# Performance work log

Measured on AMD Instinct MI355X. Metric: run time of the kernel, lower is better.

The kernel has to match this reference:

```python
import jax, jax.numpy as jnp
import numpy as np

N_PROP = 2048
N_CLS = 81  # background + 80 foreground classes
IMG_W, IMG_H = 1333.0, 800.0
SCORE_THRESH = 0.05
NMS_THRESH = 0.5
DET_PER_IMG = 100
BBOX_CLIP = float(np.log(1000.0 / 16.0))
TO_REMOVE = 1.0


def setup_inputs() -> dict:
    key = jax.random.key(0)
    k1, k2, k3, k4, k5, k6 = jax.random.split(key, 6)
    class_logits = jax.random.normal(k1, (N_PROP, N_CLS), jnp.float32)
    box_regression = jax.random.normal(k2, (N_PROP, N_CLS * 4), jnp.float32)
    # valid xyxy proposals inside the image
    x1 = jax.random.uniform(k3, (N_PROP,), jnp.float32, 0.0, IMG_W * 0.7)
    y1 = jax.random.uniform(k4, (N_PROP,), jnp.float32, 0.0, IMG_H * 0.7)
    w = jax.random.uniform(k5, (N_PROP,), jnp.float32, 16.0, IMG_W * 0.3)
    h = jax.random.uniform(k6, (N_PROP,), jnp.float32, 16.0, IMG_H * 0.3)
    proposals = jnp.stack([x1, y1, x1 + w, y1 + h], axis=-1)
    return {"class_logits": class_logits, "box_regression": box_regression, "proposals": proposals}


def decode_boxes(reg, props):
    # BoxCoder.decode with weights (10,10,5,5); reg: [N, C*4] -> [N, C, 4]
    widths = props[:, 2] - props[:, 0] + TO_REMOVE
    heights = props[:, 3] - props[:, 1] + TO_REMOVE
    ctr_x = props[:, 0] + 0.5 * widths
    ctr_y = props[:, 1] + 0.5 * heights
    r = reg.reshape(reg.shape[0], -1, 4)
    dx = r[..., 0] / 10.0
    dy = r[..., 1] / 10.0
    dw = jnp.minimum(r[..., 2] / 5.0, BBOX_CLIP)
    dh = jnp.minimum(r[..., 3] / 5.0, BBOX_CLIP)
    pcx = dx * widths[:, None] + ctr_x[:, None]
    pcy = dy * heights[:, None] + ctr_y[:, None]
    pw = jnp.exp(dw) * widths[:, None]
    ph = jnp.exp(dh) * heights[:, None]
    return jnp.stack([pcx - 0.5 * pw, pcy - 0.5 * ph,
                      pcx + 0.5 * pw - TO_REMOVE, pcy + 0.5 * ph - TO_REMOVE], axis=-1)


def pairwise_iou(b):
    # b: [N,4] xyxy -> [N,N] IoU with +1 pixel convention
    area = (b[:, 2] - b[:, 0] + TO_REMOVE) * (b[:, 3] - b[:, 1] + TO_REMOVE)
    lt = jnp.maximum(b[:, None, :2], b[None, :, :2])
    rb = jnp.minimum(b[:, None, 2:], b[None, :, 2:])
    wh = jnp.clip(rb - lt + TO_REMOVE, 0.0)
    inter = wh[..., 0] * wh[..., 1]
    return inter / (area[:, None] + area[None, :] - inter)


def nms_keep(boxes, scores, valid, thresh):
    # returns boolean keep mask (fixed shape) equivalent to greedy NMS on valid boxes
    n = scores.shape[0]
    order = jnp.argsort(-scores)
    b = boxes[order]
    v = valid[order]
    iou = pairwise_iou(b)  # [N,N]
    idx = jnp.arange(n)

    def step(suppressed, inp):
        row, vi, i = inp
        keep_i = vi & jnp.logical_not(suppressed[i])
        suppressed = suppressed | (keep_i & (row > thresh) & (idx > i))
        return suppressed, keep_i

    _, keep_sorted = jax.lax.scan(step, jnp.zeros(n, bool), (iou, v, idx))
    return jnp.zeros(n, bool).at[order].set(keep_sorted)


def _forward(class_logits, box_regression, proposals):
    probs = jax.nn.softmax(class_logits, axis=-1)          # [N, C]
    boxes = decode_boxes(box_regression, proposals)        # [N, C, 4]
    # clip_to_image (remove_empty=False)
    boxes = jnp.stack([jnp.clip(boxes[..., 0], 0.0, IMG_W - TO_REMOVE),
                       jnp.clip(boxes[..., 1], 0.0, IMG_H - TO_REMOVE),
                       jnp.clip(boxes[..., 2], 0.0, IMG_W - TO_REMOVE),
                       jnp.clip(boxes[..., 3], 0.0, IMG_H - TO_REMOVE)], axis=-1)
    # drop background class 0; class-major layout [C-1, N, ...]
    boxes_c = jnp.transpose(boxes[:, 1:, :], (1, 0, 2))    # [C-1, N, 4]
    scores_c = probs[:, 1:].T                              # [C-1, N]
    valid = scores_c > SCORE_THRESH
    keep = jax.vmap(nms_keep, in_axes=(0, 0, 0, None))(boxes_c, scores_c, valid, NMS_THRESH)
    masked = jnp.where(keep, scores_c, -1.0)               # invalid -> below any prob
    flat_scores = masked.reshape(-1)                       # [(C-1)*N]
    _, top_idx = jax.lax.top_k(flat_scores, DET_PER_IMG)
    out_scores = flat_scores[top_idx]
    out_boxes = boxes_c.reshape(-1, 4)[top_idx]
    out_labels = top_idx // N_PROP + 1                     # class labels in [1, C-1]
    return out_boxes, out_scores, out_labels


def reference(class_logits, box_regression, proposals):
    return _forward(class_logits, box_regression, proposals)
```

## Files before the change

### kernel.cpp

```cpp
#include <hip/hip_runtime.h>
#include <math.h>

#define NPROP 2048
#define NCLS 81
#define NFG 80
#define CAP 512
#define TOPC 100
#define CPAD 16
#define NB 1152
#define BMIN 0x7A99


#define LDS_FENCE() do { __builtin_amdgcn_wave_barrier(); \
    asm volatile("s_waitcnt lgkmcnt(0)" ::: "memory");     \
    __builtin_amdgcn_wave_barrier(); } while (0)

__device__ __forceinline__ void decode_clip(const float* __restrict__ props,
                                            const float* __restrict__ reg,
                                            int p, int cls, float out[4]) {
    float px1 = props[p * 4 + 0], py1 = props[p * 4 + 1];
    float px2 = props[p * 4 + 2], py2 = props[p * 4 + 3];
    float w = px2 - px1 + 1.0f;
    float h = py2 - py1 + 1.0f;
    float cx = px1 + 0.5f * w;
    float cy = py1 + 0.5f * h;
    const float* r = reg + (size_t)p * (NCLS * 4) + cls * 4;
    float dx = r[0] / 10.0f;
    float dy = r[1] / 10.0f;
    float dw = fminf(r[2] / 5.0f, 4.135166556742356f);
    float dh = fminf(r[3] / 5.0f, 4.135166556742356f);
    float pcx = dx * w + cx;
    float pcy = dy * h + cy;
    float pw = expf(dw) * w;
    float ph = expf(dh) * h;
    float x1 = pcx - 0.5f * pw;
    float y1 = pcy - 0.5f * ph;
    float x2 = pcx + 0.5f * pw - 1.0f;
    float y2 = pcy + 0.5f * ph - 1.0f;
    out[0] = fminf(fmaxf(x1, 0.0f), 1332.0f);
    out[1] = fminf(fmaxf(y1, 0.0f), 799.0f);
    out[2] = fminf(fmaxf(x2, 0.0f), 1332.0f);
    out[3] = fminf(fmaxf(y2, 0.0f), 799.0f);
}

__global__ __launch_bounds__(256) void softmax_scatter(const float* __restrict__ logits,
                                                       int* __restrict__ ccnt,
                                                       unsigned long long* __restrict__ cand) {
    int gw = (blockIdx.x * blockDim.x + threadIdx.x) >> 6;
    int lane = threadIdx.x & 63;
    if (gw >= NPROP) return;
    const float* row = logits + (size_t)gw * NCLS;
    float a = row[lane];
    bool hasb = (lane + 64) < NCLS;
    float b = hasb ? row[lane + 64] : -INFINITY;
    float m = fmaxf(a, b);
    #pragma unroll
    for (int s = 32; s; s >>= 1) m = fmaxf(m, __shfl_xor(m, s));
    float ea = expf(a - m);
    float eb = hasb ? expf(b - m) : 0.0f;
    float sum = ea + eb;
    #pragma unroll
    for (int s = 32; s; s >>= 1) sum += __shfl_xor(sum, s);
    float pa = ea / sum;
    float pb = eb / sum;
    unsigned int np = (unsigned int)(~gw);
    if (lane != 0 && pa > 0.05f) {
        int c = lane - 1;
        int pos = atomicAdd(&ccnt[c * CPAD], 1);
        if (pos < CAP)
            cand[c * CAP + pos] =
                ((unsigned long long)__float_as_uint(pa) << 32) | np;
    }
    if (hasb && pb > 0.05f) {
        int c = lane + 63;
        int pos = atomicAdd(&ccnt[c * CPAD], 1);
        if (pos < CAP)
            cand[c * CAP + pos] =
                ((unsigned long long)__float_as_uint(pb) << 32) | np;
    }
}

__global__ __launch_bounds__(64) void nms_kernel(const int* __restrict__ ccnt,
                                                 const unsigned long long* __restrict__ cand,
                                                 const float* __restrict__ props,
                                                 const float* __restrict__ reg,
                                                 int* __restrict__ scnt,
                                                 unsigned long long* __restrict__ surv) {
    const int c = blockIdx.x;
    const int lane = threadIdx.x;
    __shared__ unsigned long long keys[CAP];
    __shared__ float4 bx[CAP];
    int M = ccnt[c * CPAD];
    if (M > CAP) M = CAP;
    if (M == 0) { if (lane == 0) scnt[c] = 0; return; }
    int S = 64;
    while (S < M) S <<= 1;

    for (int i = lane; i < S; i += 64)
        keys[i] = (i < M) ? cand[c * CAP + i] : 0ULL;
    LDS_FENCE();

    for (int k = 2; k <= S; k <<= 1) {
        for (int j = k >> 1; j > 0; j >>= 1) {
            for (int i = lane; i < S; i += 64) {
                int l = i ^ j;
                if (l > i) {
                    unsigned long long A = keys[i], B = keys[l];
                    bool dir = ((i & k) == 0);
                    if ((A < B) == dir) { keys[i] = B; keys[l] = A; }
                }
            }
            LDS_FENCE();
        }
    }

    float4 myb[8];
    #pragma unroll
    for (int ns = 0; ns < 8; ++ns) {
        int idx = lane + ns * 64;
        if (idx < M) {
            unsigned long long key = keys[idx];
            int p = (int)(~(unsigned int)key);
            float b4[4];
            decode_clip(props, reg, p, c + 1, b4);
            float4 f = make_float4(b4[0], b4[1], b4[2], b4[3]);
            myb[ns] = f;
            bx[idx] = f;
        }
    }
    LDS_FENCE();

    unsigned int my_sup = 0u;
    for (int i = 0; i < M; ++i) {
        int owner = i & 63, slot = i >> 6;
        unsigned int os = __shfl(my_sup, owner);
        if ((os >> slot) & 1u) continue;
        float4 bi = bx[i];
        float ai = (bi.z - bi.x + 1.0f) * (bi.w - bi.y + 1.0f);
        #pragma unroll
        for (int ns = 0; ns < 8; ++ns) {
            int j = lane + ns * 64;
            if (j < M && j > i) {
                float4 bj = myb[ns];
                float aj = (bj.z - bj.x + 1.0f) * (bj.w - bj.y + 1.0f);
                float ltx = fmaxf(bi.x, bj.x), lty = fmaxf(bi.y, bj.y);
                float rbx = fminf(bi.z, bj.z), rby = fminf(bi.w, bj.w);
                float iw = fmaxf(rbx - ltx + 1.0f, 0.0f);
                float ih = fmaxf(rby - lty + 1.0f, 0.0f);
                float inter = iw * ih;
                float iou = inter / (ai + aj - inter);
                if (iou > 0.5f) my_sup |= (1u << ns);
            }
        }
    }

    int base = 0;
    #pragma unroll
    for (int ns = 0; ns < 8; ++ns) {
        if (ns * 64 >= M) break;
        int j = lane + ns * 64;
        bool keep = (j < M) && !((my_sup >> ns) & 1u);
        unsigned long long mask = __ballot(keep);
        if (keep) {
            int pos = base + __popcll(mask & ((1ULL << lane) - 1ULL));
            unsigned long long key = keys[j];
            int p = (int)(~(unsigned int)key);
            unsigned int flat = (unsigned int)(c * NPROP + p);
            surv[c * CAP + pos] =
                (key & 0xFFFFFFFF00000000ULL) | (unsigned int)(~flat);
        }
        base += __popcll(mask);
    }
    if (lane == 0) scnt[c] = base;
}

__global__ __launch_bounds__(256) void topk_kernel(const int* __restrict__ scnt,
                                                   const unsigned long long* __restrict__ surv,
                                                   const float* __restrict__ props,
                                                   const float* __restrict__ reg,
                                                   float* __restrict__ out) {
    __shared__ unsigned int hist[NB];
    __shared__ unsigned long long comp[1024];
    __shared__ int s_n[NFG];
    __shared__ int sB;
    __shared__ int compN;
    const int tid = threadIdx.x;

    for (int i = tid; i < NB; i += 256) hist[i] = 0u;
    if (tid < NFG) {
        int k = scnt[tid];
        s_n[tid] = (k > TOPC) ? TOPC : k;
    }
    if (tid == 0) compN = 0;
    __syncthreads();

    for (int idx = tid; idx < NFG * TOPC; idx += 256) {
        int cc = idx / TOPC, i = idx - cc * TOPC;
        if (i < s_n[cc]) {
            unsigned long long key = surv[cc * CAP + i];
            int b = (int)(((unsigned int)(key >> 32)) >> 15) - BMIN;
            b = b < 0 ? 0 : (b >= NB ? NB - 1 : b);
            atomicAdd(&hist[b], 1u);
        }
    }
    __syncthreads();

    if (tid < 64) {
        int lane = tid;
        int running = 0, Bstar = 0;
        bool found = false;
        for (int chunk = NB - 64; chunk >= 0; chunk -= 64) {
            int b = chunk + 63 - lane;
            int s = (int)hist[b];
            #pragma unroll
            for (int d = 1; d < 64; d <<= 1) {
                int o = __shfl_up(s, d);
                if (lane >= d) s += o;
            }
            int cum = running + s;
            unsigned long long m = __ballot(cum >= TOPC);
            if (m != 0ULL) {
                int l = (int)__ffsll((unsigned long long)m) - 1;
                Bstar = chunk + 63 - l;
                found = true;
                break;
            }
            running += __shfl(s, 63);
        }
        if (!found) Bstar = 0;
        if (lane == 0) sB = Bstar;
    }
    __syncthreads();
    int Bstar = sB;

    for (int idx = tid; idx < NFG * TOPC; idx += 256) {
        int cc = idx / TOPC, i = idx - cc * TOPC;
        if (i < s_n[cc]) {
            unsigned long long key = surv[cc * CAP + i];
            int b = (int)(((unsigned int)(key >> 32)) >> 15) - BMIN;
            b = b < 0 ? 0 : (b >= NB ? NB - 1 : b);
            if (b >= Bstar) {
                int pos = atomicAdd(&compN, 1);
                if (pos < 1024) comp[pos] = key;
            }
        }
    }
    __syncthreads();
    int K = compN;
    if (K > 1024) K = 1024;
    int P = 128;
    while (P < K) P <<= 1;
    for (int i = K + tid; i < P; i += 256) comp[i] = 0ULL;
    __syncthreads();

    if (tid < 64) {
        for (int k = 2; k <= P; k <<= 1) {
            for (int j = k >> 1; j > 0; j >>= 1) {
                for (int i = tid; i < P; i += 64) {
                    int l = i ^ j;
                    if (l > i) {
                        unsigned long long A = comp[i], B = comp[l];
                        bool dir = ((i & k) == 0);
                        if ((A < B) == dir) { comp[i] = B; comp[l] = A; }
                    }
                }
                LDS_FENCE();
            }
        }
    }
    __syncthreads();

    if (tid < TOPC) {
        unsigned long long key = comp[tid];
        float score;
        int flat;
        if (key == 0ULL) {
            score = -1.0f;
            flat = tid;
        } else {
            score = __uint_as_float((unsigned int)(key >> 32));
            flat = (int)(~(unsigned int)key);
        }
        int cc = flat >> 11;
        int p = flat & (NPROP - 1);
        float b4[4];
        decode_clip(props, reg, p, cc + 1, b4);
        out[tid * 4 + 0] = b4[0];
        out[tid * 4 + 1] = b4[1];
        out[tid * 4 + 2] = b4[2];
        out[tid * 4 + 3] = b4[3];
        out[400 + tid] = score;
        out[500 + tid] = (float)(cc + 1);
    }
}

extern "C" void kernel_launch(void* const* d_in, const int* in_sizes, int n_in,
                              void* d_out, int out_size, void* d_ws, size_t ws_size,
                              hipStream_t stream) {
    const float* logits = (const float*)d_in[0];
    const float* reg    = (const float*)d_in[1];
    const float* props  = (const float*)d_in[2];
    float* out = (float*)d_out;

    int* ccnt = (int*)d_ws;
    int* scnt = (int*)((char*)d_ws + 5120);
    unsigned long long* cand = (unsigned long long*)((char*)d_ws + 5440);
    unsigned long long* surv = (unsigned long long*)((char*)d_ws + 333120);

    hipMemsetAsync(d_ws, 0, 5120, stream);
    hipLaunchKernelGGL(softmax_scatter, dim3((NPROP * 64) / 256), dim3(256), 0, stream,
                       logits, ccnt, cand);
    hipLaunchKernelGGL(nms_kernel, dim3(NFG), dim3(64), 0, stream,
                       ccnt, cand, props, reg, scnt, surv);
    hipLaunchKernelGGL(topk_kernel, dim3(1), dim3(256), 0, stream,
                       scnt, surv, props, reg, out);
}
```

Before: 131.7 us.

## Fuse softmax, per-class NMS and top-k into one persistent kernel with grid barriers

```diff
diff --git a/kernel.cpp b/kernel.cpp
--- a/kernel.cpp
+++ b/kernel.cpp
@@ -4,6 +4,7 @@
 #define NPROP 2048
 #define NCLS 81
 #define NFG 80
+#define NBLK 80
 #define CAP 512
 #define TOPC 100
 #define CPAD 16
@@ -14,6 +15,26 @@
 #define LDS_FENCE() do { __builtin_amdgcn_wave_barrier(); \
     asm volatile("s_waitcnt lgkmcnt(0)" ::: "memory");     \
     __builtin_amdgcn_wave_barrier(); } while (0)
+
+__device__ __forceinline__ void grid_arrive(int* bar) {
+    __syncthreads();
+    if (threadIdx.x == 0) {
+        __threadfence();
+        atomicAdd(bar, 1);
+    }
+}
+
+__device__ __forceinline__ void grid_wait(const int* bar, int target) {
+    if (threadIdx.x == 0) {
+        int guard = 0;
+        while (__hip_atomic_load(bar, __ATOMIC_ACQUIRE,
+                                 __HIP_MEMORY_SCOPE_AGENT) < target) {
+            if (++guard > (1 << 24)) break;
+        }
+    }
+    __syncthreads();
+    __threadfence();
+}
 
 __device__ __forceinline__ void decode_clip(const float* __restrict__ props,
                                             const float* __restrict__ reg,
@@ -43,148 +64,153 @@
     out[3] = fminf(fmaxf(y2, 0.0f), 799.0f);
 }
 
-__global__ __launch_bounds__(256) void softmax_scatter(const float* __restrict__ logits,
-                                                       int* __restrict__ ccnt,
-                                                       unsigned long long* __restrict__ cand) {
-    int gw = (blockIdx.x * blockDim.x + threadIdx.x) >> 6;
-    int lane = threadIdx.x & 63;
-    if (gw >= NPROP) return;
-    const float* row = logits + (size_t)gw * NCLS;
-    float a = row[lane];
-    bool hasb = (lane + 64) < NCLS;
-    float b = hasb ? row[lane + 64] : -INFINITY;
-    float m = fmaxf(a, b);
-    #pragma unroll
-    for (int s = 32; s; s >>= 1) m = fmaxf(m, __shfl_xor(m, s));
-    float ea = expf(a - m);
-    float eb = hasb ? expf(b - m) : 0.0f;
-    float sum = ea + eb;
-    #pragma unroll
-    for (int s = 32; s; s >>= 1) sum += __shfl_xor(sum, s);
-    float pa = ea / sum;
-    float pb = eb / sum;
-    unsigned int np = (unsigned int)(~gw);
-    if (lane != 0 && pa > 0.05f) {
-        int c = lane - 1;
-        int pos = atomicAdd(&ccnt[c * CPAD], 1);
-        if (pos < CAP)
-            cand[c * CAP + pos] =
-                ((unsigned long long)__float_as_uint(pa) << 32) | np;
-    }
-    if (hasb && pb > 0.05f) {
-        int c = lane + 63;
-        int pos = atomicAdd(&ccnt[c * CPAD], 1);
-        if (pos < CAP)
-            cand[c * CAP + pos] =
-                ((unsigned long long)__float_as_uint(pb) << 32) | np;
-    }
-}
-
-__global__ __launch_bounds__(64) void nms_kernel(const int* __restrict__ ccnt,
-                                                 const unsigned long long* __restrict__ cand,
-                                                 const float* __restrict__ props,
-                                                 const float* __restrict__ reg,
-                                                 int* __restrict__ scnt,
-                                                 unsigned long long* __restrict__ surv) {
-    const int c = blockIdx.x;
-    const int lane = threadIdx.x;
+__global__ __launch_bounds__(256) void fused_postproc(const float* __restrict__ logits,
+                                                      const float* __restrict__ reg,
+                                                      const float* __restrict__ props,
+                                                      int* __restrict__ ccnt,
+                                                      int* __restrict__ bar,
+                                                      int* __restrict__ scnt,
+                                                      unsigned long long* __restrict__ cand,
+                                                      unsigned long long* __restrict__ surv,
+                                                      float* __restrict__ out) {
+    const int tid = threadIdx.x;
+    const int lane = tid & 63;
+    const int bw = tid >> 6;
+
     __shared__ unsigned long long keys[CAP];
-    __shared__ float4 bx[CAP];
-    int M = ccnt[c * CPAD];
-    if (M > CAP) M = CAP;
-    if (M == 0) { if (lane == 0) scnt[c] = 0; return; }
-    int S = 64;
-    while (S < M) S <<= 1;
-
-    for (int i = lane; i < S; i += 64)
-        keys[i] = (i < M) ? cand[c * CAP + i] : 0ULL;
-    LDS_FENCE();
-
-    for (int k = 2; k <= S; k <<= 1) {
-        for (int j = k >> 1; j > 0; j >>= 1) {
-            for (int i = lane; i < S; i += 64) {
-                int l = i ^ j;
-                if (l > i) {
-                    unsigned long long A = keys[i], B = keys[l];
-                    bool dir = ((i & k) == 0);
-                    if ((A < B) == dir) { keys[i] = B; keys[l] = A; }
-                }
-            }
-            LDS_FENCE();
-        }
-    }
-
-    float4 myb[8];
-    #pragma unroll
-    for (int ns = 0; ns < 8; ++ns) {
-        int idx = lane + ns * 64;
-        if (idx < M) {
-            unsigned long long key = keys[idx];
-            int p = (int)(~(unsigned int)key);
-            float b4[4];
-            decode_clip(props, reg, p, c + 1, b4);
-            float4 f = make_float4(b4[0], b4[1], b4[2], b4[3]);
-            myb[ns] = f;
-            bx[idx] = f;
-        }
-    }
-    LDS_FENCE();
-
-    unsigned int my_sup = 0u;
-    for (int i = 0; i < M; ++i) {
-        int owner = i & 63, slot = i >> 6;
-        unsigned int os = __shfl(my_sup, owner);
-        if ((os >> slot) & 1u) continue;
-        float4 bi = bx[i];
-        float ai = (bi.z - bi.x + 1.0f) * (bi.w - bi.y + 1.0f);
-        #pragma unroll
-        for (int ns = 0; ns < 8; ++ns) {
-            int j = lane + ns * 64;
-            if (j < M && j > i) {
-                float4 bj = myb[ns];
-                float aj = (bj.z - bj.x + 1.0f) * (bj.w - bj.y + 1.0f);
-                float ltx = fmaxf(bi.x, bj.x), lty = fmaxf(bi.y, bj.y);
-                float rbx = fminf(bi.z, bj.z), rby = fminf(bi.w, bj.w);
-                float iw = fmaxf(rbx - ltx + 1.0f, 0.0f);
-                float ih = fmaxf(rby - lty + 1.0f, 0.0f);
-                float inter = iw * ih;
-                float iou = inter / (ai + aj - inter);
-                if (iou > 0.5f) my_sup |= (1u << ns);
-            }
-        }
-    }
-
-    int base = 0;
-    #pragma unroll
-    for (int ns = 0; ns < 8; ++ns) {
-        if (ns * 64 >= M) break;
-        int j = lane + ns * 64;
-        bool keep = (j < M) && !((my_sup >> ns) & 1u);
-        unsigned long long mask = __ballot(keep);
-        if (keep) {
-            int pos = base + __popcll(mask & ((1ULL << lane) - 1ULL));
-            unsigned long long key = keys[j];
-            int p = (int)(~(unsigned int)key);
-            unsigned int flat = (unsigned int)(c * NPROP + p);
-            surv[c * CAP + pos] =
-                (key & 0xFFFFFFFF00000000ULL) | (unsigned int)(~flat);
-        }
-        base += __popcll(mask);
-    }
-    if (lane == 0) scnt[c] = base;
-}
-
-__global__ __launch_bounds__(256) void topk_kernel(const int* __restrict__ scnt,
-                                                   const unsigned long long* __restrict__ surv,
-                                                   const float* __restrict__ props,
-                                                   const float* __restrict__ reg,
-                                                   float* __restrict__ out) {
+    __shared__ float4 bxs[CAP];
     __shared__ unsigned int hist[NB];
     __shared__ unsigned long long comp[1024];
     __shared__ int s_n[NFG];
     __shared__ int sB;
     __shared__ int compN;
-    const int tid = threadIdx.x;
+
+    for (int row = blockIdx.x * 4 + bw; row < NPROP; row += NBLK * 4) {
+        const float* lrow = logits + (size_t)row * NCLS;
+        float a = lrow[lane];
+        bool hasb = (lane + 64) < NCLS;
+        float b = hasb ? lrow[lane + 64] : -INFINITY;
+        float m = fmaxf(a, b);
+        #pragma unroll
+        for (int s = 32; s; s >>= 1) m = fmaxf(m, __shfl_xor(m, s));
+        float ea = expf(a - m);
+        float eb = hasb ? expf(b - m) : 0.0f;
+        float sum = ea + eb;
+        #pragma unroll
+        for (int s = 32; s; s >>= 1) sum += __shfl_xor(sum, s);
+        float pa = ea / sum;
+        float pb = eb / sum;
+        unsigned int np = (unsigned int)(~row);
+        if (lane != 0 && pa > 0.05f) {
+            int c = lane - 1;
+            int pos = atomicAdd(&ccnt[c * CPAD], 1);
+            if (pos < CAP)
+                cand[c * CAP + pos] =
+                    ((unsigned long long)__float_as_uint(pa) << 32) | np;
+        }
+        if (hasb && pb > 0.05f) {
+            int c = lane + 63;
+            int pos = atomicAdd(&ccnt[c * CPAD], 1);
+            if (pos < CAP)
+                cand[c * CAP + pos] =
+                    ((unsigned long long)__float_as_uint(pb) << 32) | np;
+        }
+    }
+
+    grid_arrive(bar);
+    grid_wait(bar, NBLK);
+
+    const int c = blockIdx.x;
+    if (bw == 0) {
+        int M = ccnt[c * CPAD];
+        if (M > CAP) M = CAP;
+        if (M > 0) {
+            int S = 64;
+            while (S < M) S <<= 1;
+            for (int i = lane; i < S; i += 64)
+                keys[i] = (i < M) ? cand[c * CAP + i] : 0ULL;
+            LDS_FENCE();
+
+            for (int k = 2; k <= S; k <<= 1) {
+                for (int j = k >> 1; j > 0; j >>= 1) {
+                    for (int i = lane; i < S; i += 64) {
+                        int l = i ^ j;
+                        if (l > i) {
+                            unsigned long long A = keys[i], B = keys[l];
+                            bool dir = ((i & k) == 0);
+                            if ((A < B) == dir) { keys[i] = B; keys[l] = A; }
+                        }
+                    }
+                    LDS_FENCE();
+                }
+            }
+
+            float4 myb[8];
+            #pragma unroll
+            for (int ns = 0; ns < 8; ++ns) {
+                int idx = lane + ns * 64;
+                if (idx < M) {
+                    unsigned long long key = keys[idx];
+                    int p = (int)(~(unsigned int)key);
+                    float b4[4];
+                    decode_clip(props, reg, p, c + 1, b4);
+                    float4 f = make_float4(b4[0], b4[1], b4[2], b4[3]);
+                    myb[ns] = f;
+                    bxs[idx] = f;
+                }
+            }
+            LDS_FENCE();
+
+            unsigned int my_sup = 0u;
+            for (int i = 0; i < M; ++i) {
+                int owner = i & 63, slot = i >> 6;
+                unsigned int os = __shfl(my_sup, owner);
+                if ((os >> slot) & 1u) continue;
+                float4 bi = bxs[i];
+                float ai = (bi.z - bi.x + 1.0f) * (bi.w - bi.y + 1.0f);
+                #pragma unroll
+                for (int ns = 0; ns < 8; ++ns) {
+                    int j = lane + ns * 64;
+                    if (j < M && j > i) {
+                        float4 bj = myb[ns];
+                        float aj = (bj.z - bj.x + 1.0f) * (bj.w - bj.y + 1.0f);
+                        float ltx = fmaxf(bi.x, bj.x), lty = fmaxf(bi.y, bj.y);
+                        float rbx = fminf(bi.z, bj.z), rby = fminf(bi.w, bj.w);
+                        float iw = fmaxf(rbx - ltx + 1.0f, 0.0f);
+                        float ih = fmaxf(rby - lty + 1.0f, 0.0f);
+                        float inter = iw * ih;
+                        float iou = inter / (ai + aj - inter);
+                        if (iou > 0.5f) my_sup |= (1u << ns);
+                    }
+                }
+            }
+
+            int base = 0;
+            #pragma unroll
+            for (int ns = 0; ns < 8; ++ns) {
+                if (ns * 64 >= M) break;
+                int j = lane + ns * 64;
+                bool keep = (j < M) && !((my_sup >> ns) & 1u);
+                unsigned long long mask = __ballot(keep);
+                if (keep) {
+                    int pos = base + __popcll(mask & ((1ULL << lane) - 1ULL));
+                    unsigned long long key = keys[j];
+                    int p = (int)(~(unsigned int)key);
+                    unsigned int flat = (unsigned int)(c * NPROP + p);
+                    surv[c * CAP + pos] =
+                        (key & 0xFFFFFFFF00000000ULL) | (unsigned int)(~flat);
+                }
+                base += __popcll(mask);
+            }
+            if (lane == 0) scnt[c] = base;
+        } else {
+            if (lane == 0) scnt[c] = 0;
+        }
+    }
+
+    grid_arrive(bar);
+    if (blockIdx.x != 0) return;
+    grid_wait(bar, 2 * NBLK);
 
     for (int i = tid; i < NB; i += 256) hist[i] = 0u;
     if (tid < NFG) {
@@ -206,16 +232,15 @@
     __syncthreads();
 
     if (tid < 64) {
-        int lane = tid;
         int running = 0, Bstar = 0;
         bool found = false;
         for (int chunk = NB - 64; chunk >= 0; chunk -= 64) {
-            int b = chunk + 63 - lane;
+            int b = chunk + 63 - tid;
             int s = (int)hist[b];
             #pragma unroll
             for (int d = 1; d < 64; d <<= 1) {
                 int o = __shfl_up(s, d);
-                if (lane >= d) s += o;
+                if (tid >= d) s += o;
             }
             int cum = running + s;
             unsigned long long m = __ballot(cum >= TOPC);
@@ -228,7 +253,7 @@
             running += __shfl(s, 63);
         }
         if (!found) Bstar = 0;
-        if (lane == 0) sB = Bstar;
+        if (tid == 0) sB = Bstar;
     }
     __syncthreads();
     int Bstar = sB;
@@ -303,15 +328,12 @@
     float* out = (float*)d_out;
 
     int* ccnt = (int*)d_ws;
-    int* scnt = (int*)((char*)d_ws + 5120);
-    unsigned long long* cand = (unsigned long long*)((char*)d_ws + 5440);
-    unsigned long long* surv = (unsigned long long*)((char*)d_ws + 333120);
-
-    hipMemsetAsync(d_ws, 0, 5120, stream);
-    hipLaunchKernelGGL(softmax_scatter, dim3((NPROP * 64) / 256), dim3(256), 0, stream,
-                       logits, ccnt, cand);
-    hipLaunchKernelGGL(nms_kernel, dim3(NFG), dim3(64), 0, stream,
-                       ccnt, cand, props, reg, scnt, surv);
-    hipLaunchKernelGGL(topk_kernel, dim3(1), dim3(256), 0, stream,
-                       scnt, surv, props, reg, out);
-}
+    int* bar  = (int*)((char*)d_ws + 5120);
+    int* scnt = (int*)((char*)d_ws + 5184);
+    unsigned long long* cand = (unsigned long long*)((char*)d_ws + 5504);
+    unsigned long long* surv = (unsigned long long*)((char*)d_ws + 333184);
+
+    hipMemsetAsync(d_ws, 0, 5184, stream);
+    hipLaunchKernelGGL(fused_postproc, dim3(NBLK), dim3(256), 0, stream,
+                       logits, reg, props, ccnt, bar, scnt, cand, surv, out);
+}
```

Result: slower. 149.2 us (+13.2%).
